# Optimization experiments

Measured on AMD Instinct MI355X. Metric: run time of the kernel, lower is better.

## Reference

```python
import jax, jax.numpy as jnp
import numpy as np
jax.config.update("jax_enable_x64", True)

N = 16384   # nodes
C = 16      # initial color vocabulary size
B = 64      # number of graphs in the batch
_rs = np.random.RandomState(42)
_MULTS = jnp.asarray((_rs.randint(1, 2 ** 62, size=C + 1).astype(np.int64) << 1) | 1)  # odd 64-bit hash multipliers


def setup_inputs() -> dict:
    key = jax.random.key(0)
    k1, k2, k3 = jax.random.split(key, 3)
    x = jax.random.randint(k1, (N,), 0, C, dtype=jnp.int64)
    adj_t = jax.random.randint(k2, (N, N), 0, 2).astype(jnp.float32)  # dense binary adjacency
    batch = jnp.sort(jax.random.randint(k3, (N,), 0, B, dtype=jnp.int64))
    return {"x": x, "adj_t": adj_t, "batch": batch}


def _wl_colors(x, adj_t):
    # One WL refinement step. The torch code hashes (own_color, sorted neighbor colors)
    # and assigns new ids by insertion order into an OrderedDict ('isolate' -> 0).
    # A sorted tuple of neighbor colors is equivalent to the neighbor color multiset,
    # which we represent as a count histogram and hash with a 64-bit wraparound
    # polynomial hash; ids are then assigned by first-occurrence (node-index) order.
    n = x.shape[0]
    onehot = jax.nn.one_hot(x, C, dtype=adj_t.dtype)                 # [N, C]
    nbr_hist = jnp.round(adj_t @ onehot).astype(jnp.int64)           # [N, C] neighbor color counts
    iso = (adj_t.sum(axis=1) + adj_t.sum(axis=0)) == 0               # isolated nodes
    h = x * _MULTS[0] + (nbr_hist * _MULTS[1:]).sum(axis=-1)         # int64 wraparound hash
    h = jnp.where(iso, jnp.int64(-(2 ** 63)), h)
    order = jnp.argsort(h)
    hs = h[order]
    new_grp = jnp.concatenate([jnp.ones((1,), bool), hs[1:] != hs[:-1]])
    gid = jnp.zeros(n, jnp.int64).at[order].set(jnp.cumsum(new_grp) - 1)   # group id per node
    first_of_grp = jax.ops.segment_min(jnp.arange(n), gid, num_segments=n)
    firsts = first_of_grp[gid]                                       # first node index with same signature
    is_first = (~iso) & (firsts == jnp.arange(n))
    rank = jnp.cumsum(is_first.astype(jnp.int64))                    # hashmap insertion order (1-based)
    return jnp.where(iso, 0, rank[firsts])                           # 'isolate' -> 0


def _histogram(colors, batch):
    # Per-graph color histogram; width padded to N+1 (max possible distinct colors)
    # for static shapes -- extra columns are zero and do not affect the L2 norm.
    num_colors = N + 1
    idx = batch * num_colors + colors
    out = jnp.zeros(B * num_colors, jnp.int64).at[idx].add(1)
    out = out.reshape(B, num_colors)[:, 1:]                          # drop 'isolate' column
    out = out.astype(jnp.float64)
    return out / jnp.linalg.norm(out, axis=-1, keepdims=True)


def reference(x, adj_t, batch):
    colors = _wl_colors(x, adj_t)          # forward's default return value
    hist = _histogram(colors, batch)       # return_embedding=True output
    return hist, colors
```

## Files before the change

### kernel.cpp

```cpp
#include <hip/hip_runtime.h>
#include <stdint.h>

#define NN 16384
#define NC 16
#define NB 64

struct Mults { unsigned long long m[17]; };


__global__ __launch_bounds__(256) void k_table(const int* __restrict__ x,
                                               unsigned long long* __restrict__ table) {
  int idx = blockIdx.x * 256 + threadIdx.x;
  int c = idx & 15, k = (idx >> 4) & 3, chunk = idx >> 6;
  unsigned long long m = 0ull;
  for (int l = 0; l < 64; ++l) {
    int col = chunk * 256 + l * 4 + k;
    if (x[col] == c) m |= (1ull << l);
  }
  table[idx] = m;
}

__global__ __launch_bounds__(256) void k_hist(const float* __restrict__ adj,
                                              const unsigned long long* __restrict__ table,
                                              int* __restrict__ nbr_hist) {
  __shared__ unsigned long long tbl[4096];
  for (int i = threadIdx.x; i < 4096; i += 256) tbl[i] = table[i];
  __syncthreads();
  int wave = threadIdx.x >> 6;
  int lane = threadIdx.x & 63;
  int row  = blockIdx.x * 4 + wave;
  const uint4* rowp = (const uint4*)(adj + (size_t)row * NN);
  int c = lane & 15, k = lane >> 4;
  const unsigned long long* tk = &tbl[k * 16 + c];
  int cnt = 0;
  for (int chunk = 0; chunk < 64; ++chunk) {
    uint4 v = rowp[chunk * 64 + lane];
    unsigned long long b0 = __ballot(v.x != 0u);
    unsigned long long b1 = __ballot(v.y != 0u);
    unsigned long long b2 = __ballot(v.z != 0u);
    unsigned long long b3 = __ballot(v.w != 0u);
    unsigned long long m = (k & 2) ? ((k & 1) ? b3 : b2) : ((k & 1) ? b1 : b0);
    cnt += __popcll(m & tk[chunk * 64]);
  }
  cnt += __shfl_xor(cnt, 16, 64);
  cnt += __shfl_xor(cnt, 32, 64);
  if (lane < 16) nbr_hist[row * 16 + lane] = cnt;
}

__global__ __launch_bounds__(256) void k_rowsum(const int* __restrict__ nbr_hist,
                                                int* __restrict__ colany,
                                                int* __restrict__ suspects,
                                                int* __restrict__ scount) {
  int i = blockIdx.x * 256 + threadIdx.x;
  int rs = 0;
  for (int c = 0; c < 16; ++c) rs += nbr_hist[i * 16 + c];
  colany[i] = 1;
  if (rs == 0) { int s = atomicAdd(scount, 1); suspects[s] = i; }
}

__global__ __launch_bounds__(256) void k_colcheck(const float* __restrict__ adj,
                                                  const int* __restrict__ suspects,
                                                  const int* __restrict__ scount,
                                                  int* __restrict__ colany) {
  __shared__ int red[256];
  int nsus = *scount;
  for (int u = blockIdx.x; u < nsus; u += gridDim.x) {
    int col = suspects[u];
    int any = 0;
    for (int r = threadIdx.x; r < NN; r += 256)
      any |= (adj[(size_t)r * NN + col] != 0.0f);
    red[threadIdx.x] = any;
    __syncthreads();
    for (int s = 128; s > 0; s >>= 1) {
      if (threadIdx.x < s) red[threadIdx.x] |= red[threadIdx.x + s];
      __syncthreads();
    }
    if (threadIdx.x == 0) colany[col] = red[0];
    __syncthreads();
  }
}

__global__ __launch_bounds__(256) void k_hash(const int* __restrict__ x,
                                              const int* __restrict__ nbr_hist,
                                              const int* __restrict__ colany,
                                              Mults M,
                                              unsigned long long* __restrict__ h,
                                              int* __restrict__ iso) {
  int i = blockIdx.x * 256 + threadIdx.x;
  unsigned long long acc = (unsigned long long)(long long)x[i] * M.m[0];
  int rs = 0;
  for (int c = 0; c < 16; ++c) {
    int v = nbr_hist[i * 16 + c];
    rs += v;
    acc += (unsigned long long)(long long)v * M.m[c + 1];
  }
  int is_iso = (rs == 0) && (colany[i] == 0);
  iso[i] = is_iso;
  h[i] = is_iso ? 0x8000000000000000ull : acc;
}

#define JC 2048
__global__ __launch_bounds__(256) void k_firsts_part(const unsigned long long* __restrict__ h,
                                                     int* __restrict__ part) {
  __shared__ unsigned long long hs[JC];
  int chunk = blockIdx.y;
  int jbase = chunk * JC;
  for (int t = threadIdx.x; t < JC; t += 256) hs[t] = h[jbase + t];
  __syncthreads();
  int i = blockIdx.x * 256 + threadIdx.x;
  unsigned long long hi = h[i];
  int best = 0x7fffffff;
  for (int jj = 0; jj < JC; ++jj) {
    if (hs[jj] == hi) best = min(best, jbase + jj);
  }
  part[chunk * NN + i] = best;
}

__global__ __launch_bounds__(256) void k_firsts_merge(const int* __restrict__ part,
                                                      int* __restrict__ firsts) {
  int i = blockIdx.x * 256 + threadIdx.x;
  int best = 0x7fffffff;
  for (int ch = 0; ch < NN / JC; ++ch) best = min(best, part[ch * NN + i]);
  firsts[i] = best;
}

__global__ __launch_bounds__(1024) void k_scan(const int* __restrict__ iso,
                                               const int* __restrict__ firsts,
                                               int* __restrict__ rank) {
  __shared__ int sums[1024];
  int t = threadIdx.x;
  int base = t * 16;
  int loc[16];
  int s = 0;
  for (int u = 0; u < 16; ++u) {
    int i = base + u;
    int isf = (!iso[i]) && (firsts[i] == i);
    s += isf;
    loc[u] = s;
  }
  sums[t] = s;
  __syncthreads();
  for (int off = 1; off < 1024; off <<= 1) {
    int add = (t >= off) ? sums[t - off] : 0;
    __syncthreads();
    sums[t] += add;
    __syncthreads();
  }
  int excl = sums[t] - s;
  for (int u = 0; u < 16; ++u) rank[base + u] = excl + loc[u];
}

__global__ __launch_bounds__(256) void k_colors(const int* __restrict__ iso,
                                                const int* __restrict__ firsts,
                                                const int* __restrict__ rank,
                                                int* __restrict__ colors,
                                                float* __restrict__ out_colors) {
  int i = blockIdx.x * 256 + threadIdx.x;
  int c = iso[i] ? 0 : rank[firsts[i]];
  colors[i] = c;
  out_colors[i] = (float)c;
}

__global__ __launch_bounds__(256) void k_count(const int* __restrict__ colors,
                                               const int* __restrict__ batch,
                                               int* __restrict__ cnt) {
  int i = blockIdx.x * 256 + threadIdx.x;
  int c = colors[i];
  if (c > 0) atomicAdd(&cnt[(size_t)batch[i] * NN + (c - 1)], 1);
}

__global__ __launch_bounds__(256) void k_norm(const int* __restrict__ cnt,
                                              float* __restrict__ out) {
  __shared__ float red[256];
  int b = blockIdx.x;
  float ss = 0.0f;
  for (int j = threadIdx.x; j < NN; j += 256) {
    float v = (float)cnt[(size_t)b * NN + j];
    ss += v * v;
  }
  red[threadIdx.x] = ss;
  __syncthreads();
  for (int s = 128; s > 0; s >>= 1) {
    if (threadIdx.x < s) red[threadIdx.x] += red[threadIdx.x + s];
    __syncthreads();
  }
  float nrm = sqrtf(red[0]);
  for (int j = threadIdx.x; j < NN; j += 256)
    out[(size_t)b * NN + j] = (float)cnt[(size_t)b * NN + j] / nrm;
}


struct MTState { uint32_t mt[624]; int idx; };

static void mt_seed(MTState& s, uint32_t seed) {
  s.mt[0] = seed;
  for (int i = 1; i < 624; ++i)
    s.mt[i] = 1812433253u * (s.mt[i - 1] ^ (s.mt[i - 1] >> 30)) + (uint32_t)i;
  s.idx = 624;
}

static uint32_t mt_next(MTState& s) {
  if (s.idx >= 624) {
    for (int i = 0; i < 624; ++i) {
      uint32_t y = (s.mt[i] & 0x80000000u) | (s.mt[(i + 1) % 624] & 0x7fffffffu);
      uint32_t nx = s.mt[(i + 397) % 624] ^ (y >> 1);
      if (y & 1u) nx ^= 2567483615u;
      s.mt[i] = nx;
    }
    s.idx = 0;
  }
  uint32_t y = s.mt[s.idx++];
  y ^= y >> 11;
  y ^= (y << 7) & 2636928640u;
  y ^= (y << 15) & 4022730752u;
  y ^= y >> 18;
  return y;
}

static uint64_t mt_next64(MTState& s) {
  uint64_t hi = mt_next(s);
  uint64_t lo = mt_next(s);
  return (hi << 32) | lo;
}


extern "C" void kernel_launch(void* const* d_in, const int* in_sizes, int n_in,
                              void* d_out, int out_size, void* d_ws, size_t ws_size,
                              hipStream_t stream) {
  const int*   x     = (const int*)d_in[0];
  const float* adj   = (const float*)d_in[1];
  const int*   batch = (const int*)d_in[2];
  float* out_hist   = (float*)d_out;
  float* out_colors = out_hist + (size_t)NB * NN;

  char* ws = (char*)d_ws;
  unsigned long long* table = (unsigned long long*)(ws + 0);
  int*                nhist = (int*)(ws + 32768);
  unsigned long long* h     = (unsigned long long*)(ws + 1081344);
  int*                part  = (int*)(ws + 1212416);
  int*                cnt   = (int*)(ws + 0);
  int* colany   = (int*)(ws + 4194304);
  int* suspects = (int*)(ws + 4259840);
  int* scount   = (int*)(ws + 4325376);
  int* iso      = (int*)(ws + 4325632);
  int* firsts   = (int*)(ws + 4391168);
  int* rank     = (int*)(ws + 4456704);
  int* colors   = (int*)(ws + 4522240);

  Mults M;
  {
    MTState st;
    mt_seed(st, 42u);
    const uint64_t mask62 = (1ull << 62) - 1ull;
    const uint64_t rng    = (1ull << 62) - 2ull;
    for (int i = 0; i < 17; ++i) {
      uint64_t v;
      do { v = mt_next64(st) & mask62; } while (v > rng);
      M.m[i] = ((1ull + v) << 1) | 1ull;
    }
  }

  hipMemsetAsync(scount, 0, 4, stream);
  k_table<<<16, 256, 0, stream>>>(x, table);
  k_hist<<<NN / 4, 256, 0, stream>>>(adj, table, nhist);
  k_rowsum<<<NN / 256, 256, 0, stream>>>(nhist, colany, suspects, scount);
  k_colcheck<<<64, 256, 0, stream>>>(adj, suspects, scount, colany);
  k_hash<<<NN / 256, 256, 0, stream>>>(x, nhist, colany, M, h, iso);
  dim3 ge(NN / 256, NN / JC);
  k_firsts_part<<<ge, 256, 0, stream>>>(h, part);
  k_firsts_merge<<<NN / 256, 256, 0, stream>>>(part, firsts);
  k_scan<<<1, 1024, 0, stream>>>(iso, firsts, rank);
  k_colors<<<NN / 256, 256, 0, stream>>>(iso, firsts, rank, colors, out_colors);
  hipMemsetAsync(cnt, 0, (size_t)NB * NN * 4, stream);
  k_count<<<NN / 256, 256, 0, stream>>>(colors, batch, cnt);
  k_norm<<<NB, 256, 0, stream>>>(cnt, out_hist);
}
```

Baseline: 1.442 ms.

## Fuse WL pipeline kernels and drop LDS table staging in histogram

Folds the row-sum, hash and iso initialization into the adjacency histogram kernel, and has the column check write iso and hash directly. The two-pass firsts computation becomes a single kernel using atomicMin, and colors plus histogram counting are merged into the scan kernel with rank held in LDS. The bitmask table is now read from global memory instead of being staged in shared memory. The aim is fewer launches and less intermediate traffic, but the large counting work now runs in a single block and per-chunk table loads come from cache.

```diff
diff --git a/kernel.cpp b/kernel.cpp
--- a/kernel.cpp
+++ b/kernel.cpp
@@ -9,7 +9,9 @@
 
 
 __global__ __launch_bounds__(256) void k_table(const int* __restrict__ x,
-                                               unsigned long long* __restrict__ table) {
+                                               unsigned long long* __restrict__ table,
+                                               int* __restrict__ scount) {
+  if (blockIdx.x == 0 && threadIdx.x == 0) *scount = 0;
   int idx = blockIdx.x * 256 + threadIdx.x;
   int c = idx & 15, k = (idx >> 4) & 3, chunk = idx >> 6;
   unsigned long long m = 0ull;
@@ -22,16 +24,20 @@
 
 __global__ __launch_bounds__(256) void k_hist(const float* __restrict__ adj,
                                               const unsigned long long* __restrict__ table,
-                                              int* __restrict__ nbr_hist) {
-  __shared__ unsigned long long tbl[4096];
-  for (int i = threadIdx.x; i < 4096; i += 256) tbl[i] = table[i];
-  __syncthreads();
+                                              const int* __restrict__ x,
+                                              Mults M,
+                                              unsigned long long* __restrict__ h,
+                                              int* __restrict__ iso,
+                                              int* __restrict__ firsts,
+                                              int* __restrict__ suspects,
+                                              int* __restrict__ scount) {
   int wave = threadIdx.x >> 6;
   int lane = threadIdx.x & 63;
   int row  = blockIdx.x * 4 + wave;
+  int xv   = x[row];
   const uint4* rowp = (const uint4*)(adj + (size_t)row * NN);
   int c = lane & 15, k = lane >> 4;
-  const unsigned long long* tk = &tbl[k * 16 + c];
+  const unsigned long long* tk = table + (k * 16 + c);
   int cnt = 0;
   for (int chunk = 0; chunk < 64; ++chunk) {
     uint4 v = rowp[chunk * 64 + lane];
@@ -44,24 +50,29 @@
   }
   cnt += __shfl_xor(cnt, 16, 64);
   cnt += __shfl_xor(cnt, 32, 64);
-  if (lane < 16) nbr_hist[row * 16 + lane] = cnt;
-}
-
-__global__ __launch_bounds__(256) void k_rowsum(const int* __restrict__ nbr_hist,
-                                                int* __restrict__ colany,
-                                                int* __restrict__ suspects,
-                                                int* __restrict__ scount) {
-  int i = blockIdx.x * 256 + threadIdx.x;
-  int rs = 0;
-  for (int c = 0; c < 16; ++c) rs += nbr_hist[i * 16 + c];
-  colany[i] = 1;
-  if (rs == 0) { int s = atomicAdd(scount, 1); suspects[s] = i; }
+  int rs = cnt;
+  rs += __shfl_xor(rs, 1, 64);
+  rs += __shfl_xor(rs, 2, 64);
+  rs += __shfl_xor(rs, 4, 64);
+  rs += __shfl_xor(rs, 8, 64);
+  unsigned long long hl = (unsigned long long)(long long)cnt * M.m[(lane & 15) + 1];
+  hl += __shfl_xor(hl, 1, 64);
+  hl += __shfl_xor(hl, 2, 64);
+  hl += __shfl_xor(hl, 4, 64);
+  hl += __shfl_xor(hl, 8, 64);
+  if (lane == 0) {
+    h[row] = hl + (unsigned long long)(long long)xv * M.m[0];
+    if (rs == 0) { int s = atomicAdd(scount, 1); suspects[s] = row; }
+  }
+  if (lane == 1) iso[row] = 0;
+  if (lane == 2) firsts[row] = 0x7fffffff;
 }
 
 __global__ __launch_bounds__(256) void k_colcheck(const float* __restrict__ adj,
                                                   const int* __restrict__ suspects,
                                                   const int* __restrict__ scount,
-                                                  int* __restrict__ colany) {
+                                                  int* __restrict__ iso,
+                                                  unsigned long long* __restrict__ h) {
   __shared__ int red[256];
   int nsus = *scount;
   for (int u = blockIdx.x; u < nsus; u += gridDim.x) {
@@ -75,36 +86,19 @@
       if (threadIdx.x < s) red[threadIdx.x] |= red[threadIdx.x + s];
       __syncthreads();
     }
-    if (threadIdx.x == 0) colany[col] = red[0];
-    __syncthreads();
-  }
-}
-
-__global__ __launch_bounds__(256) void k_hash(const int* __restrict__ x,
-                                              const int* __restrict__ nbr_hist,
-                                              const int* __restrict__ colany,
-                                              Mults M,
-                                              unsigned long long* __restrict__ h,
-                                              int* __restrict__ iso) {
-  int i = blockIdx.x * 256 + threadIdx.x;
-  unsigned long long acc = (unsigned long long)(long long)x[i] * M.m[0];
-  int rs = 0;
-  for (int c = 0; c < 16; ++c) {
-    int v = nbr_hist[i * 16 + c];
-    rs += v;
-    acc += (unsigned long long)(long long)v * M.m[c + 1];
-  }
-  int is_iso = (rs == 0) && (colany[i] == 0);
-  iso[i] = is_iso;
-  h[i] = is_iso ? 0x8000000000000000ull : acc;
+    if (threadIdx.x == 0 && red[0] == 0) {
+      iso[col] = 1;
+      h[col] = 0x8000000000000000ull;
+    }
+    __syncthreads();
+  }
 }
 
 #define JC 2048
-__global__ __launch_bounds__(256) void k_firsts_part(const unsigned long long* __restrict__ h,
-                                                     int* __restrict__ part) {
+__global__ __launch_bounds__(256) void k_firsts(const unsigned long long* __restrict__ h,
+                                                int* __restrict__ firsts) {
   __shared__ unsigned long long hs[JC];
-  int chunk = blockIdx.y;
-  int jbase = chunk * JC;
+  int jbase = blockIdx.y * JC;
   for (int t = threadIdx.x; t < JC; t += 256) hs[t] = h[jbase + t];
   __syncthreads();
   int i = blockIdx.x * 256 + threadIdx.x;
@@ -113,20 +107,15 @@
   for (int jj = 0; jj < JC; ++jj) {
     if (hs[jj] == hi) best = min(best, jbase + jj);
   }
-  part[chunk * NN + i] = best;
-}
-
-__global__ __launch_bounds__(256) void k_firsts_merge(const int* __restrict__ part,
-                                                      int* __restrict__ firsts) {
-  int i = blockIdx.x * 256 + threadIdx.x;
-  int best = 0x7fffffff;
-  for (int ch = 0; ch < NN / JC; ++ch) best = min(best, part[ch * NN + i]);
-  firsts[i] = best;
+  if (best < 0x7fffffff) atomicMin(&firsts[i], best);
 }
 
 __global__ __launch_bounds__(1024) void k_scan(const int* __restrict__ iso,
                                                const int* __restrict__ firsts,
-                                               int* __restrict__ rank) {
+                                               const int* __restrict__ batch,
+                                               float* __restrict__ out_colors,
+                                               int* __restrict__ cnt) {
+  __shared__ int rank_lds[NN];
   __shared__ int sums[1024];
   int t = threadIdx.x;
   int base = t * 16;
@@ -147,26 +136,14 @@
     __syncthreads();
   }
   int excl = sums[t] - s;
-  for (int u = 0; u < 16; ++u) rank[base + u] = excl + loc[u];
-}
-
-__global__ __launch_bounds__(256) void k_colors(const int* __restrict__ iso,
-                                                const int* __restrict__ firsts,
-                                                const int* __restrict__ rank,
-                                                int* __restrict__ colors,
-                                                float* __restrict__ out_colors) {
-  int i = blockIdx.x * 256 + threadIdx.x;
-  int c = iso[i] ? 0 : rank[firsts[i]];
-  colors[i] = c;
-  out_colors[i] = (float)c;
-}
-
-__global__ __launch_bounds__(256) void k_count(const int* __restrict__ colors,
-                                               const int* __restrict__ batch,
-                                               int* __restrict__ cnt) {
-  int i = blockIdx.x * 256 + threadIdx.x;
-  int c = colors[i];
-  if (c > 0) atomicAdd(&cnt[(size_t)batch[i] * NN + (c - 1)], 1);
+  for (int u = 0; u < 16; ++u) rank_lds[base + u] = excl + loc[u];
+  __syncthreads();
+  for (int u = 0; u < 16; ++u) {
+    int i = base + u;
+    int c = iso[i] ? 0 : rank_lds[firsts[i]];
+    out_colors[i] = (float)c;
+    if (c > 0) atomicAdd(&cnt[(size_t)batch[i] * NN + (c - 1)], 1);
+  }
 }
 
 __global__ __launch_bounds__(256) void k_norm(const int* __restrict__ cnt,
@@ -234,18 +211,13 @@
   float* out_colors = out_hist + (size_t)NB * NN;
 
   char* ws = (char*)d_ws;
-  unsigned long long* table = (unsigned long long*)(ws + 0);
-  int*                nhist = (int*)(ws + 32768);
-  unsigned long long* h     = (unsigned long long*)(ws + 1081344);
-  int*                part  = (int*)(ws + 1212416);
-  int*                cnt   = (int*)(ws + 0);
-  int* colany   = (int*)(ws + 4194304);
-  int* suspects = (int*)(ws + 4259840);
-  int* scount   = (int*)(ws + 4325376);
-  int* iso      = (int*)(ws + 4325632);
-  int* firsts   = (int*)(ws + 4391168);
-  int* rank     = (int*)(ws + 4456704);
-  int* colors   = (int*)(ws + 4522240);
+  int*                cnt      = (int*)(ws + 0);
+  int*                scount   = (int*)(ws + 4194304);
+  int*                suspects = (int*)(ws + 4194560);
+  unsigned long long* h        = (unsigned long long*)(ws + 4260096);
+  int*                iso      = (int*)(ws + 4391168);
+  int*                firsts   = (int*)(ws + 4456704);
+  unsigned long long* table    = (unsigned long long*)(ws + 4522240);
 
   Mults M;
   {
@@ -260,18 +232,12 @@
     }
   }
 
-  hipMemsetAsync(scount, 0, 4, stream);
-  k_table<<<16, 256, 0, stream>>>(x, table);
-  k_hist<<<NN / 4, 256, 0, stream>>>(adj, table, nhist);
-  k_rowsum<<<NN / 256, 256, 0, stream>>>(nhist, colany, suspects, scount);
-  k_colcheck<<<64, 256, 0, stream>>>(adj, suspects, scount, colany);
-  k_hash<<<NN / 256, 256, 0, stream>>>(x, nhist, colany, M, h, iso);
-  dim3 ge(NN / 256, NN / JC);
-  k_firsts_part<<<ge, 256, 0, stream>>>(h, part);
-  k_firsts_merge<<<NN / 256, 256, 0, stream>>>(part, firsts);
-  k_scan<<<1, 1024, 0, stream>>>(iso, firsts, rank);
-  k_colors<<<NN / 256, 256, 0, stream>>>(iso, firsts, rank, colors, out_colors);
   hipMemsetAsync(cnt, 0, (size_t)NB * NN * 4, stream);
-  k_count<<<NN / 256, 256, 0, stream>>>(colors, batch, cnt);
+  k_table<<<16, 256, 0, stream>>>(x, table, scount);
+  k_hist<<<NN / 4, 256, 0, stream>>>(adj, table, x, M, h, iso, firsts, suspects, scount);
+  k_colcheck<<<64, 256, 0, stream>>>(adj, suspects, scount, iso, h);
+  dim3 gf(NN / 256, NN / JC);
+  k_firsts<<<gf, 256, 0, stream>>>(h, firsts);
+  k_scan<<<1, 1024, 0, stream>>>(iso, firsts, batch, out_colors, cnt);
   k_norm<<<NB, 256, 0, stream>>>(cnt, out_hist);
 }
```

Measured after the change: 1.469 ms. About the same (+1.9%).
